# Kernel optimization log

Hardware: AMD Instinct MI355X
Metric: run time of the kernel (lower is better)

The kernel has to match this reference:

```python
import jax, jax.numpy as jnp
import numpy as np

N_NODES = 200000
N_EDGES = 3200000
F_IN = 128
CH = 32
N_GRAPHS = 1024
N_LABELS = 17


def setup_inputs() -> dict:
    key = jax.random.key(0)
    ks = jax.random.split(key, 16)
    x = jax.random.normal(ks[0], (N_NODES, F_IN), dtype=jnp.float32)
    a_row = jax.random.randint(ks[1], (N_EDGES,), 0, N_NODES, dtype=jnp.int64)
    a_col = jax.random.randint(ks[2], (N_EDGES,), 0, N_NODES, dtype=jnp.int64)
    a_val = jax.random.uniform(ks[3], (N_EDGES,), dtype=jnp.float32)
    seg = jnp.sort(jax.random.randint(ks[4], (N_NODES,), 0, N_GRAPHS, dtype=jnp.int64))
    def glorot(k, fan_in, fan_out):
        lim = np.sqrt(6.0 / (fan_in + fan_out)).astype(np.float32)
        return jax.random.uniform(k, (fan_in, fan_out), dtype=jnp.float32, minval=-lim, maxval=lim)
    params = {
        'W1_1': glorot(ks[5], F_IN, CH), 'W2_1': glorot(ks[6], F_IN, CH), 'b_1': jnp.zeros((CH,), jnp.float32),
        'W1_2': glorot(ks[7], CH, CH),   'W2_2': glorot(ks[8], CH, CH),   'b_2': jnp.zeros((CH,), jnp.float32),
        'W1_3': glorot(ks[9], CH, CH),   'W2_3': glorot(ks[10], CH, CH),  'b_3': jnp.zeros((CH,), jnp.float32),
        'Wd': glorot(ks[11], CH, N_LABELS), 'bd': jnp.zeros((N_LABELS,), jnp.float32),
    }
    return dict(x=x, a_row=a_row, a_col=a_col, a_val=a_val, seg=seg, **params)


def _gcs_conv(x, a_row, a_col, a_val, W1, W2, b):
    # A @ X via gather(col) -> weight -> scatter-add(row)
    msgs = a_val[:, None] * x[a_col]            # [E, F]
    agg = jax.ops.segment_sum(msgs, a_row, num_segments=N_NODES)  # [N, F]
    return jax.nn.relu(agg @ W1 + x @ W2 + b)


def reference(x, a_row, a_col, a_val, seg,
              W1_1, W2_1, b_1, W1_2, W2_2, b_2, W1_3, W2_3, b_3, Wd, bd):
    h = _gcs_conv(x, a_row, a_col, a_val, W1_1, W2_1, b_1)
    h = _gcs_conv(h, a_row, a_col, a_val, W1_2, W2_2, b_2)
    h = _gcs_conv(h, a_row, a_col, a_val, W1_3, W2_3, b_3)
    # GlobalAvgPool over batch index i: segment mean per graph
    sums = jax.ops.segment_sum(h, seg, num_segments=N_GRAPHS)          # [G, CH]
    cnts = jax.ops.segment_sum(jnp.ones((N_NODES,), h.dtype), seg, num_segments=N_GRAPHS)
    pooled = sums / jnp.maximum(cnts, 1.0)[:, None]
    return jax.nn.softmax(pooled @ Wd + bd, axis=-1)
```

## Files before the change

### kernel.cpp

```cpp
#include <hip/hip_runtime.h>
#include <cstdint>

#define N_NODES 200000
#define N_EDGES 3200000
#define F_IN 128
#define CH 32
#define N_GRAPHS 1024
#define N_LABELS 17

#define BROWS 512
#define NBUCK ((N_NODES + BROWS - 1) / BROWS)
#define CAP 10240
#define EPB 8192
#define NB_D1 ((N_NODES + 255) / 256)
#define NB_A ((N_EDGES + EPB - 1) / EPB)

typedef unsigned int uint32;
typedef unsigned short u16;

#define TSCALE 16.f

__device__ __forceinline__ u16 f2bf(float f) {
  unsigned int u = __float_as_uint(f);
  u = (u + 0x7FFFu + ((u >> 16) & 1u)) >> 16;
  return (u16)u;
}
__device__ __forceinline__ float bf2f(u16 h) {
  return __uint_as_float(((unsigned int)h) << 16);
}
__device__ __forceinline__ signed char f2q8(float f) {
  float qf = fmaxf(-127.f, fminf(127.f, rintf(f * TSCALE)));
  return (signed char)(int)qf;
}


__global__ __launch_bounds__(256) void k_d1A(const float* __restrict__ x,
                                             const float* __restrict__ W1,
                                             const float* __restrict__ W2,
                                             signed char* __restrict__ tout,
                                             u16* __restrict__ sout,
                                             const int* __restrict__ arow,
                                             const int* __restrict__ acol,
                                             const float* __restrict__ aval,
                                             int* __restrict__ bucketCur,
                                             unsigned long long* __restrict__ records) {
  __shared__ int cnt[NBUCK];
  __shared__ int base[NBUCK];
  int blk = blockIdx.x;
  int t = threadIdx.x;
  if (blk < NB_D1) {
    int i = blk * 256 + t;
    if (i >= N_NODES) return;
    const float* xr = x + (size_t)i * F_IN;
    float acc1[CH], acc2[CH];
#pragma unroll
    for (int c = 0; c < CH; c++) { acc1[c] = 0.f; acc2[c] = 0.f; }
#pragma unroll 8
    for (int k = 0; k < F_IN; k += 4) {
      float4 xv = *(const float4*)(xr + k);
      float xk[4] = {xv.x, xv.y, xv.z, xv.w};
#pragma unroll
      for (int kk = 0; kk < 4; kk++) {
        float xval = xk[kk];
        const float* w1r = W1 + (size_t)(k + kk) * CH;
        const float* w2r = W2 + (size_t)(k + kk) * CH;
#pragma unroll
        for (int c = 0; c < CH; c++) {
          acc1[c] = fmaf(xval, w1r[c], acc1[c]);
          acc2[c] = fmaf(xval, w2r[c], acc2[c]);
        }
      }
    }
    uint32* tp = (uint32*)(tout + (size_t)i * CH);
#pragma unroll
    for (int c = 0; c < CH; c += 4) {
      uint32 p = ((uint32)(unsigned char)f2q8(acc1[c])) |
                 ((uint32)(unsigned char)f2q8(acc1[c + 1]) << 8) |
                 ((uint32)(unsigned char)f2q8(acc1[c + 2]) << 16) |
                 ((uint32)(unsigned char)f2q8(acc1[c + 3]) << 24);
      tp[c >> 2] = p;
    }
    uint32* sp = (uint32*)(sout + (size_t)i * CH);
#pragma unroll
    for (int c = 0; c < CH; c += 2) {
      sp[c >> 1] = (uint32)f2bf(acc2[c]) | ((uint32)f2bf(acc2[c + 1]) << 16);
    }
    return;
  }
  int ab = blk - NB_D1;
  for (int i = t; i < NBUCK; i += 256) cnt[i] = 0;
  __syncthreads();
  int e0 = ab * EPB;
  int e1 = e0 + EPB; if (e1 > N_EDGES) e1 = N_EDGES;
  for (int e = e0 + t; e < e1; e += 256) atomicAdd(&cnt[arow[e] >> 9], 1);
  __syncthreads();
  for (int i = t; i < NBUCK; i += 256) {
    int n = cnt[i];
    base[i] = n ? atomicAdd(&bucketCur[i], n) : 0;
    cnt[i] = 0;
  }
  __syncthreads();
  for (int e = e0 + t; e < e1; e += 256) {
    int r = arow[e];
    int b = r >> 9;
    int p = atomicAdd(&cnt[b], 1) + base[b];
    if (p < CAP) {
      unsigned int hi = ((unsigned int)(r & 511) << 18) | (unsigned int)acol[e];
      unsigned long long rec = ((unsigned long long)hi << 32) |
                               (unsigned int)__float_as_int(aval[e]);
      records[(size_t)b * CAP + p] = rec;
    }
  }
}


__global__ __launch_bounds__(512) void k_passB(const int* __restrict__ bucketCur,
                                               const unsigned long long* __restrict__ records,
                                               int2* __restrict__ rowinfo,
                                               uint32* __restrict__ edges) {
  __shared__ int cnt[BROWS];
  __shared__ int sc[BROWS];
  __shared__ int cur[BROWS];
  int b = blockIdx.x;
  int t = threadIdx.x;
  int nrec = bucketCur[b]; if (nrec > CAP) nrec = CAP;
  const unsigned long long* rp = records + (size_t)b * CAP;
  cnt[t] = 0;
  __syncthreads();
  for (int i = t; i < nrec; i += 512) {
    unsigned int hi = (unsigned int)(rp[i] >> 32);
    atomicAdd(&cnt[hi >> 18], 1);
  }
  __syncthreads();
  sc[t] = cnt[t];
  __syncthreads();
  for (int d = 1; d < BROWS; d <<= 1) {
    int v = (t >= d) ? sc[t - d] : 0;
    __syncthreads();
    sc[t] += v;
    __syncthreads();
  }
  int pre = sc[t] - cnt[t];
  cur[t] = pre;
  int r = b * BROWS + t;
  if (r < N_NODES) rowinfo[r] = make_int2(b * CAP + pre, cnt[t]);
  __syncthreads();
  for (int i = t; i < nrec; i += 512) {
    unsigned long long rec = rp[i];
    unsigned int hi = (unsigned int)(rec >> 32);
    int rl = hi >> 18;
    unsigned int col = hi & 0x3FFFFu;
    float val = __int_as_float((int)(unsigned int)rec);
    int q = (int)fmaf(val, 16383.f, 0.5f);
    q = q < 0 ? 0 : (q > 16383 ? 16383 : q);
    int p = atomicAdd(&cur[rl], 1);
    edges[(size_t)b * CAP + p] = (col << 14) | (unsigned int)q;
  }
}


template <int MODE>
__global__ __launch_bounds__(256) void k_gcs(const int2* __restrict__ rowinfo,
                                             const uint32* __restrict__ edges,
                                             const signed char* __restrict__ tin,
                                             u16* __restrict__ sio,
                                             const float* __restrict__ bias,
                                             const float* __restrict__ W1n,
                                             const float* __restrict__ W2n,
                                             signed char* __restrict__ tout,
                                             float* __restrict__ hout) {
  int gid = blockIdx.x * blockDim.x + threadIdx.x;
  int node = gid >> 5;
  int c = gid & 31;
  if (node >= N_NODES) return;
  int2 ri = rowinfo[node];
  const uint32* ep = edges + ri.x;
  int n = ri.y;
  float s = bf2f(sio[((size_t)node << 5) + c]);
  float a[4] = {0.f, 0.f, 0.f, 0.f};
  for (int e = 0; e < n; e += 16) {
    uint32 d[16];
    int g[16];
    float v[16];
#pragma unroll
    for (int j = 0; j < 16; j++) {
      int ij = e + j;
      d[j] = ep[ij < n ? ij : n - 1];
    }
#pragma unroll
    for (int j = 0; j < 16; j++) {
      g[j] = (int)tin[((size_t)(d[j] >> 14) << 5) + c];
    }
#pragma unroll
    for (int j = 0; j < 16; j++) {
      v[j] = (e + j < n) ? (float)(d[j] & 0x3FFFu) : 0.f;
    }
#pragma unroll
    for (int j = 0; j < 16; j++) {
      a[j & 3] = fmaf(v[j], (float)g[j], a[j & 3]);
    }
  }
  float acc = ((a[0] + a[1]) + (a[2] + a[3])) * (1.f / (16383.f * TSCALE));
  float h = fmaxf(acc + s + bias[c], 0.f);
  if (MODE == 1) {
    hout[((size_t)node << 5) + c] = h;
  } else {
    float m1 = 0.f, m2 = 0.f;
#pragma unroll
    for (int k = 0; k < CH; k++) {
      float hk = __shfl(h, k, 32);
      m1 = fmaf(hk, W1n[k * CH + c], m1);
      m2 = fmaf(hk, W2n[k * CH + c], m2);
    }
    tout[((size_t)node << 5) + c] = f2q8(m1);
    sio[((size_t)node << 5) + c] = f2bf(m2);
  }
}


__global__ void k_head(const float* __restrict__ h, const int* __restrict__ seg,
                       const float* __restrict__ Wd, const float* __restrict__ bd,
                       float* __restrict__ out) {
  int g = blockIdx.x;
  int t = threadIdx.x;
  __shared__ float red[64];
  __shared__ float pooled[CH];
  __shared__ float logits[N_LABELS];
  int lo, hi;
  {
    int l = 0, r = N_NODES;
    while (l < r) { int m = (l + r) >> 1; if (seg[m] < g) l = m + 1; else r = m; }
    lo = l;
  }
  {
    int l = 0, r = N_NODES;
    while (l < r) { int m = (l + r) >> 1; if (seg[m] < g + 1) l = m + 1; else r = m; }
    hi = l;
  }
  float acc = 0.f;
  int c = t & 31, half = t >> 5;
  for (int i = lo + half; i < hi; i += 2) acc += h[(size_t)i * CH + c];
  red[t] = acc;
  __syncthreads();
  if (t < CH) {
    float cnt = (float)((hi - lo) > 0 ? (hi - lo) : 1);
    pooled[t] = (red[t] + red[t + 32]) / cnt;
  }
  __syncthreads();
  if (t < N_LABELS) {
    float a = bd[t];
#pragma unroll
    for (int k = 0; k < CH; k++) a = fmaf(pooled[k], Wd[k * N_LABELS + t], a);
    logits[t] = a;
  }
  __syncthreads();
  if (t == 0) {
    float mx = logits[0];
    for (int j = 1; j < N_LABELS; j++) mx = fmaxf(mx, logits[j]);
    float ssum = 0.f;
    float e[N_LABELS];
    for (int j = 0; j < N_LABELS; j++) { e[j] = expf(logits[j] - mx); ssum += e[j]; }
    float inv = 1.f / ssum;
    for (int j = 0; j < N_LABELS; j++) out[(size_t)g * N_LABELS + j] = e[j] * inv;
  }
}


extern "C" void kernel_launch(void* const* d_in, const int* in_sizes, int n_in,
                              void* d_out, int out_size, void* d_ws, size_t ws_size,
                              hipStream_t stream) {
  const float* x    = (const float*)d_in[0];
  const int*   arow = (const int*)d_in[1];
  const int*   acol = (const int*)d_in[2];
  const float* aval = (const float*)d_in[3];
  const int*   seg  = (const int*)d_in[4];
  const float* W1_1 = (const float*)d_in[5];
  const float* W2_1 = (const float*)d_in[6];
  const float* b_1  = (const float*)d_in[7];
  const float* W1_2 = (const float*)d_in[8];
  const float* W2_2 = (const float*)d_in[9];
  const float* b_2  = (const float*)d_in[10];
  const float* W1_3 = (const float*)d_in[11];
  const float* W2_3 = (const float*)d_in[12];
  const float* b_3  = (const float*)d_in[13];
  const float* Wd   = (const float*)d_in[14];
  const float* bd   = (const float*)d_in[15];
  float* out = (float*)d_out;

  char* w = (char*)d_ws;
  signed char* tA = (signed char*)w; w += (size_t)N_NODES * CH;
  signed char* tB = (signed char*)w; w += (size_t)N_NODES * CH;
  u16* sS = (u16*)w;                 w += (size_t)N_NODES * CH * 2;
  float* hbuf = (float*)w;           w += (size_t)N_NODES * CH * 4;
  uint32* edges = (uint32*)w;        w += (size_t)NBUCK * CAP * 4;
  int2* rowinfo = (int2*)w;          w += (size_t)N_NODES * 8;
  int* bucketCur = (int*)w;          w += 4096;
  unsigned long long* records = (unsigned long long*)w;
  w += (size_t)NBUCK * CAP * 8;

  hipMemsetAsync(bucketCur, 0, (size_t)NBUCK * 4, stream);

  k_d1A<<<NB_D1 + NB_A, 256, 0, stream>>>(x, W1_1, W2_1, tA, sS,
                                          arow, acol, aval, bucketCur, records);

  k_passB<<<NBUCK, 512, 0, stream>>>(bucketCur, records, rowinfo, edges);

  const int GCS_GRID = (N_NODES * 32 + 255) / 256;
  k_gcs<0><<<GCS_GRID, 256, 0, stream>>>(rowinfo, edges, tA, sS, b_1, W1_2, W2_2, tB, nullptr);
  k_gcs<0><<<GCS_GRID, 256, 0, stream>>>(rowinfo, edges, tB, sS, b_2, W1_3, W2_3, tA, nullptr);
  k_gcs<1><<<GCS_GRID, 256, 0, stream>>>(rowinfo, edges, tA, sS, b_3, nullptr, nullptr, nullptr, hbuf);

  k_head<<<N_GRAPHS, 64, 0, stream>>>(hbuf, seg, Wd, bd, out);
}
```

Baseline: 425.5 us.

## Split fused dense/bucket kernel, alias records buffer, shuffle-broadcast edge loads in gcs

Splits the combined first-layer dense transform and edge-bucketing kernel into two separate launches. The bucket records buffer now aliases the start of the workspace, which the dense kernel later overwrites, so the workspace shrinks and the footprint can stay more cache-resident. In the gather kernel, each lane loads one edge word and the 16 words are broadcast with warp shuffles instead of every lane loading all 16. The split gives up concurrency between the dense and bucketing phases, and shuffles add ALU work in place of redundant loads.

```diff
diff --git a/kernel.cpp b/kernel.cpp
--- a/kernel.cpp
+++ b/kernel.cpp
@@ -12,8 +12,6 @@
 #define NBUCK ((N_NODES + BROWS - 1) / BROWS)
 #define CAP 10240
 #define EPB 8192
-#define NB_D1 ((N_NODES + 255) / 256)
-#define NB_A ((N_EDGES + EPB - 1) / EPB)
 
 typedef unsigned int uint32;
 typedef unsigned short u16;
@@ -34,63 +32,17 @@
 }
 
 
-__global__ __launch_bounds__(256) void k_d1A(const float* __restrict__ x,
-                                             const float* __restrict__ W1,
-                                             const float* __restrict__ W2,
-                                             signed char* __restrict__ tout,
-                                             u16* __restrict__ sout,
-                                             const int* __restrict__ arow,
-                                             const int* __restrict__ acol,
-                                             const float* __restrict__ aval,
-                                             int* __restrict__ bucketCur,
-                                             unsigned long long* __restrict__ records) {
+__global__ __launch_bounds__(256) void k_passA(const int* __restrict__ arow,
+                                               const int* __restrict__ acol,
+                                               const float* __restrict__ aval,
+                                               int* __restrict__ bucketCur,
+                                               unsigned long long* __restrict__ records) {
   __shared__ int cnt[NBUCK];
   __shared__ int base[NBUCK];
-  int blk = blockIdx.x;
   int t = threadIdx.x;
-  if (blk < NB_D1) {
-    int i = blk * 256 + t;
-    if (i >= N_NODES) return;
-    const float* xr = x + (size_t)i * F_IN;
-    float acc1[CH], acc2[CH];
-#pragma unroll
-    for (int c = 0; c < CH; c++) { acc1[c] = 0.f; acc2[c] = 0.f; }
-#pragma unroll 8
-    for (int k = 0; k < F_IN; k += 4) {
-      float4 xv = *(const float4*)(xr + k);
-      float xk[4] = {xv.x, xv.y, xv.z, xv.w};
-#pragma unroll
-      for (int kk = 0; kk < 4; kk++) {
-        float xval = xk[kk];
-        const float* w1r = W1 + (size_t)(k + kk) * CH;
-        const float* w2r = W2 + (size_t)(k + kk) * CH;
-#pragma unroll
-        for (int c = 0; c < CH; c++) {
-          acc1[c] = fmaf(xval, w1r[c], acc1[c]);
-          acc2[c] = fmaf(xval, w2r[c], acc2[c]);
-        }
-      }
-    }
-    uint32* tp = (uint32*)(tout + (size_t)i * CH);
-#pragma unroll
-    for (int c = 0; c < CH; c += 4) {
-      uint32 p = ((uint32)(unsigned char)f2q8(acc1[c])) |
-                 ((uint32)(unsigned char)f2q8(acc1[c + 1]) << 8) |
-                 ((uint32)(unsigned char)f2q8(acc1[c + 2]) << 16) |
-                 ((uint32)(unsigned char)f2q8(acc1[c + 3]) << 24);
-      tp[c >> 2] = p;
-    }
-    uint32* sp = (uint32*)(sout + (size_t)i * CH);
-#pragma unroll
-    for (int c = 0; c < CH; c += 2) {
-      sp[c >> 1] = (uint32)f2bf(acc2[c]) | ((uint32)f2bf(acc2[c + 1]) << 16);
-    }
-    return;
-  }
-  int ab = blk - NB_D1;
   for (int i = t; i < NBUCK; i += 256) cnt[i] = 0;
   __syncthreads();
-  int e0 = ab * EPB;
+  int e0 = blockIdx.x * EPB;
   int e1 = e0 + EPB; if (e1 > N_EDGES) e1 = N_EDGES;
   for (int e = e0 + t; e < e1; e += 256) atomicAdd(&cnt[arow[e] >> 9], 1);
   __syncthreads();
@@ -155,6 +107,50 @@
     q = q < 0 ? 0 : (q > 16383 ? 16383 : q);
     int p = atomicAdd(&cur[rl], 1);
     edges[(size_t)b * CAP + p] = (col << 14) | (unsigned int)q;
+  }
+}
+
+
+__global__ __launch_bounds__(256) void k_dense1(const float* __restrict__ x,
+                                                const float* __restrict__ W1,
+                                                const float* __restrict__ W2,
+                                                signed char* __restrict__ tout,
+                                                u16* __restrict__ sout) {
+  int i = blockIdx.x * blockDim.x + threadIdx.x;
+  if (i >= N_NODES) return;
+  const float* xr = x + (size_t)i * F_IN;
+  float acc1[CH], acc2[CH];
+#pragma unroll
+  for (int c = 0; c < CH; c++) { acc1[c] = 0.f; acc2[c] = 0.f; }
+#pragma unroll 8
+  for (int k = 0; k < F_IN; k += 4) {
+    float4 xv = *(const float4*)(xr + k);
+    float xk[4] = {xv.x, xv.y, xv.z, xv.w};
+#pragma unroll
+    for (int kk = 0; kk < 4; kk++) {
+      float xval = xk[kk];
+      const float* w1r = W1 + (size_t)(k + kk) * CH;
+      const float* w2r = W2 + (size_t)(k + kk) * CH;
+#pragma unroll
+      for (int c = 0; c < CH; c++) {
+        acc1[c] = fmaf(xval, w1r[c], acc1[c]);
+        acc2[c] = fmaf(xval, w2r[c], acc2[c]);
+      }
+    }
+  }
+  uint32* tp = (uint32*)(tout + (size_t)i * CH);
+#pragma unroll
+  for (int c = 0; c < CH; c += 4) {
+    uint32 p = ((uint32)(unsigned char)f2q8(acc1[c])) |
+               ((uint32)(unsigned char)f2q8(acc1[c + 1]) << 8) |
+               ((uint32)(unsigned char)f2q8(acc1[c + 2]) << 16) |
+               ((uint32)(unsigned char)f2q8(acc1[c + 3]) << 24);
+    tp[c >> 2] = p;
+  }
+  uint32* sp = (uint32*)(sout + (size_t)i * CH);
+#pragma unroll
+  for (int c = 0; c < CH; c += 2) {
+    sp[c >> 1] = (uint32)f2bf(acc2[c]) | ((uint32)f2bf(acc2[c + 1]) << 16);
   }
 }
 
@@ -177,30 +173,28 @@
   const uint32* ep = edges + ri.x;
   int n = ri.y;
   float s = bf2f(sio[((size_t)node << 5) + c]);
-  float a[4] = {0.f, 0.f, 0.f, 0.f};
+  float a0 = 0.f, a1 = 0.f, a2 = 0.f, a3 = 0.f;
   for (int e = 0; e < n; e += 16) {
+    int el = e + (c & 15);
+    uint32 me = ep[el < n ? el : n - 1];
     uint32 d[16];
+#pragma unroll
+    for (int j = 0; j < 16; j++) d[j] = __shfl(me, j, 32) ;
     int g[16];
-    float v[16];
-#pragma unroll
-    for (int j = 0; j < 16; j++) {
-      int ij = e + j;
-      d[j] = ep[ij < n ? ij : n - 1];
-    }
 #pragma unroll
     for (int j = 0; j < 16; j++) {
       g[j] = (int)tin[((size_t)(d[j] >> 14) << 5) + c];
     }
 #pragma unroll
     for (int j = 0; j < 16; j++) {
-      v[j] = (e + j < n) ? (float)(d[j] & 0x3FFFu) : 0.f;
-    }
-#pragma unroll
-    for (int j = 0; j < 16; j++) {
-      a[j & 3] = fmaf(v[j], (float)g[j], a[j & 3]);
-    }
-  }
-  float acc = ((a[0] + a[1]) + (a[2] + a[3])) * (1.f / (16383.f * TSCALE));
+      float v = (e + j < n) ? (float)(d[j] & 0x3FFFu) : 0.f;
+      if ((j & 3) == 0) a0 = fmaf(v, (float)g[j], a0);
+      else if ((j & 3) == 1) a1 = fmaf(v, (float)g[j], a1);
+      else if ((j & 3) == 2) a2 = fmaf(v, (float)g[j], a2);
+      else a3 = fmaf(v, (float)g[j], a3);
+    }
+  }
+  float acc = ((a0 + a1) + (a2 + a3)) * (1.f / (16383.f * TSCALE));
   float h = fmaxf(acc + s + bias[c], 0.f);
   if (MODE == 1) {
     hout[((size_t)node << 5) + c] = h;
@@ -295,15 +289,13 @@
   uint32* edges = (uint32*)w;        w += (size_t)NBUCK * CAP * 4;
   int2* rowinfo = (int2*)w;          w += (size_t)N_NODES * 8;
   int* bucketCur = (int*)w;          w += 4096;
-  unsigned long long* records = (unsigned long long*)w;
-  w += (size_t)NBUCK * CAP * 8;
+  unsigned long long* records = (unsigned long long*)d_ws;
 
   hipMemsetAsync(bucketCur, 0, (size_t)NBUCK * 4, stream);
-
-  k_d1A<<<NB_D1 + NB_A, 256, 0, stream>>>(x, W1_1, W2_1, tA, sS,
-                                          arow, acol, aval, bucketCur, records);
-
+  k_passA<<<(N_EDGES + EPB - 1) / EPB, 256, 0, stream>>>(arow, acol, aval, bucketCur, records);
   k_passB<<<NBUCK, 512, 0, stream>>>(bucketCur, records, rowinfo, edges);
+
+  k_dense1<<<(N_NODES + 255) / 256, 256, 0, stream>>>(x, W1_1, W2_1, tA, sS);
 
   const int GCS_GRID = (N_NODES * 32 + 255) / 256;
   k_gcs<0><<<GCS_GRID, 256, 0, stream>>>(rowinfo, edges, tA, sS, b_1, W1_2, W2_2, tB, nullptr);
```

Measured after the change: 411.3 us. -3.3%, faster.
